# Optimization experiments

Measured on AMD Instinct MI355X. Metric: run time of the kernel, lower is better.

The kernel has to match this reference:

```python
import jax, jax.numpy as jnp
import numpy as np

B, D, L, H = 8192, 1024, 64, 256

def setup_inputs() -> dict:
    key = jax.random.key(0)
    k_x, k_w1, k_b1, k_w2, k_b2 = jax.random.split(key, 5)
    # Stacked per-label parameters (equivalent to L independent 2-layer MLPs)
    lim1 = 1.0 / np.sqrt(D)
    lim2 = 1.0 / np.sqrt(H)
    return {
        "x": jax.random.normal(k_x, (B, D), dtype=jnp.float32),
        "W1": jax.random.uniform(k_w1, (L, D, H), dtype=jnp.float32, minval=-lim1, maxval=lim1),
        "b1": jax.random.uniform(k_b1, (L, H), dtype=jnp.float32, minval=-lim1, maxval=lim1),
        "W2": jax.random.uniform(k_w2, (L, H), dtype=jnp.float32, minval=-lim2, maxval=lim2),
        "b2": jax.random.uniform(k_b2, (L,), dtype=jnp.float32, minval=-lim2, maxval=lim2),
    }

def reference(x, W1, b1, W2, b2):
    # h: [B, L, H] = relu(x @ W1_l + b1_l) for every label l, as one batched GEMM
    h = jax.nn.relu(jnp.einsum('bd,ldh->blh', x, W1) + b1[None, :, :])
    # out: [B, L] = h_l @ W2_l + b2_l  (second Linear has output dim 1, squeezed)
    out = jnp.einsum('blh,lh->bl', h, W2) + b2[None, :]
    return out
```

## Files before the change

kernel.cpp:

```cpp
#include <hip/hip_runtime.h>
#include <stdint.h>

#define B_SZ 8192
#define D_SZ 1024
#define L_SZ 64
#define H_SZ 256

#define BM 128
#define BN 256
#define BK 32
#define NTILE (D_SZ / BK)

typedef __attribute__((ext_vector_type(8))) __bf16 bf16x8;
typedef __attribute__((ext_vector_type(4))) float f32x4;

typedef __attribute__((address_space(1))) void as1_void;
typedef __attribute__((address_space(3))) void as3_void;

static __device__ __forceinline__ void gload_lds16(const void* g, void* l) {
    __builtin_amdgcn_global_load_lds((as1_void*)g, (as3_void*)l, 16, 0, 0);
}

static __device__ __forceinline__ unsigned short f2bf(float f) {
    uint32_t u = __builtin_bit_cast(uint32_t, f);
    u += 0x7fffu + ((u >> 16) & 1u);
    return (unsigned short)(u >> 16);
}

__global__ void cvt_x_kernel(const float* __restrict__ x, unsigned short* __restrict__ xb) {
    int i = blockIdx.x * blockDim.x + threadIdx.x;
    const float4 v = reinterpret_cast<const float4*>(x)[i];
    ushort4 o;
    o.x = f2bf(v.x); o.y = f2bf(v.y); o.z = f2bf(v.z); o.w = f2bf(v.w);
    reinterpret_cast<ushort4*>(xb)[i] = o;
}

__global__ void transpose_w1_kernel(const float* __restrict__ w1, unsigned short* __restrict__ w1t) {
    __shared__ float tile[64][65];
    int b = blockIdx.x;
    int l  = b >> 6;
    int dt = (b >> 2) & 15;
    int ht = b & 3;
    int tx = threadIdx.x & 63;
    int ty = threadIdx.x >> 6;
    const float* src = w1 + (size_t)l * (D_SZ * H_SZ);
    #pragma unroll
    for (int r = 0; r < 64; r += 4)
        tile[r + ty][tx] = src[(size_t)(dt * 64 + r + ty) * H_SZ + ht * 64 + tx];
    __syncthreads();
    unsigned short* dst = w1t + (size_t)l * (H_SZ * D_SZ);
    #pragma unroll
    for (int r = 0; r < 64; r += 4)
        dst[(size_t)(ht * 64 + r + ty) * D_SZ + dt * 64 + tx] = f2bf(tile[tx][r + ty]);
}


#define SBAR asm volatile("s_barrier" ::: "memory")
#define VMW(n) asm volatile("s_waitcnt vmcnt(" #n ")" ::: "memory")

#define STAGE(t, bi) do { \
    const size_t koff = (size_t)(t) * BK; \
    gload_lds16(aSrcG + koff,    (char*)&ldsA[bi][0] + tid * 16); \
    gload_lds16(bSrcG0 + koff,   (char*)&ldsB[bi][0] + tid * 16); \
    gload_lds16(bSrcG1 + koff,   (char*)&ldsB[bi][0] + 8192 + tid * 16); \
} while(0)

#define COMPUTE(bi) do { \
    bf16x8 af[4], bv[4]; \
    _Pragma("unroll") for (int m = 0; m < 4; ++m) { \
        const int row = wr * 64 + m * 16 + rl; \
        const int slot = gq ^ ((row >> 1) & 3); \
        af[m] = *reinterpret_cast<const bf16x8*>( \
            reinterpret_cast<const char*>(&ldsA[bi][0]) + row * 64 + slot * 16); \
    } \
    _Pragma("unroll") for (int n = 0; n < 4; ++n) { \
        const int row = wc * 64 + n * 16 + rl; \
        const int slot = gq ^ ((row >> 1) & 3); \
        bv[n] = *reinterpret_cast<const bf16x8*>( \
            reinterpret_cast<const char*>(&ldsB[bi][0]) + row * 64 + slot * 16); \
    } \
    __builtin_amdgcn_s_setprio(1); \
    _Pragma("unroll") for (int m = 0; m < 4; ++m) \
    _Pragma("unroll") for (int n = 0; n < 4; ++n) \
        acc[m][n] = __builtin_amdgcn_mfma_f32_16x16x32_bf16(af[m], bv[n], acc[m][n], 0, 0, 0); \
    __builtin_amdgcn_s_setprio(0); \
} while(0)

__global__ __launch_bounds__(512, 4) void ffn_gemm_kernel(
    const unsigned short* __restrict__ xb,
    const unsigned short* __restrict__ w1t,
    const float* __restrict__ b1,
    const float* __restrict__ w2,
    const float* __restrict__ b2,
    float* __restrict__ out)
{
    __shared__ unsigned short ldsA[3][BM * BK];
    __shared__ unsigned short ldsB[3][BN * BK];
    __shared__ float partLds[2][64][4];

    const int bid = blockIdx.x;
    const int wg  = ((bid & 7) << 9) + (bid >> 3);
    const int l   = wg >> 6;
    const int m0  = (wg & 63) * BM;

    const int tid  = threadIdx.x;
    const int wid  = tid >> 6;
    const int lane = tid & 63;
    const int wr   = wid >> 2;
    const int wc   = wid & 3;
    const int gq   = lane >> 4;
    const int rl   = lane & 15;

    const int arow = tid >> 2;
    const int aslt = tid & 3;
    const unsigned short* aSrcG =
        xb + (size_t)(m0 + arow) * D_SZ + (aslt ^ ((arow >> 1) & 3)) * 8;
    const int brow0 = tid >> 2;
    const unsigned short* bSrcG0 =
        w1t + ((size_t)l * H_SZ + brow0) * D_SZ + ((tid & 3) ^ ((brow0 >> 1) & 3)) * 8;
    const int q1 = 512 + tid;
    const int brow1 = q1 >> 2;
    const unsigned short* bSrcG1 =
        w1t + ((size_t)l * H_SZ + brow1) * D_SZ + ((q1 & 3) ^ ((brow1 >> 1) & 3)) * 8;

    f32x4 acc[4][4];
    #pragma unroll
    for (int m = 0; m < 4; ++m)
        #pragma unroll
        for (int n = 0; n < 4; ++n) {
            acc[m][n][0] = 0.f; acc[m][n][1] = 0.f;
            acc[m][n][2] = 0.f; acc[m][n][3] = 0.f;
        }

    STAGE(0, 0); STAGE(1, 1);
    VMW(3);
    SBAR;

    #pragma unroll 1
    for (int tt = 0; tt < 30; tt += 3) {
        STAGE(tt + 2, 2); VMW(6); SBAR; COMPUTE(0); SBAR;
        STAGE(tt + 3, 0); VMW(6); SBAR; COMPUTE(1); SBAR;
        STAGE(tt + 4, 1); VMW(6); SBAR; COMPUTE(2); SBAR;
    }
    VMW(3); SBAR; COMPUTE(0); SBAR;
    VMW(0); SBAR; COMPUTE(1);

    float b1v[4], w2v[4];
    #pragma unroll
    for (int n = 0; n < 4; ++n) {
        const int col = wc * 64 + n * 16 + rl;
        b1v[n] = b1[l * H_SZ + col];
        w2v[n] = w2[l * H_SZ + col];
    }
    const float b2v = b2[l];
    #pragma unroll
    for (int m = 0; m < 4; ++m) {
        #pragma unroll
        for (int r = 0; r < 4; ++r) {
            float p = 0.f;
            #pragma unroll
            for (int n = 0; n < 4; ++n) {
                float v = acc[m][n][r] + b1v[n];
                v = fmaxf(v, 0.f);
                p += v * w2v[n];
            }
            p += __shfl_xor(p, 1);
            p += __shfl_xor(p, 2);
            p += __shfl_xor(p, 4);
            p += __shfl_xor(p, 8);
            if (rl == 0)
                partLds[wr][m * 16 + gq * 4 + r][wc] = p;
        }
    }
    __syncthreads();
    if (tid < BM) {
        float s = b2v;
        #pragma unroll
        for (int w = 0; w < 4; ++w) s += partLds[tid >> 6][tid & 63][w];
        out[(size_t)(m0 + tid) * L_SZ + l] = s;
    }
}

extern "C" void kernel_launch(void* const* d_in, const int* in_sizes, int n_in,
                              void* d_out, int out_size, void* d_ws, size_t ws_size,
                              hipStream_t stream) {
    const float* x  = (const float*)d_in[0];
    const float* W1 = (const float*)d_in[1];
    const float* b1 = (const float*)d_in[2];
    const float* W2 = (const float*)d_in[3];
    const float* b2 = (const float*)d_in[4];
    float* out = (float*)d_out;

    unsigned short* xb  = (unsigned short*)d_ws;
    unsigned short* w1t = xb + (size_t)B_SZ * D_SZ;

    cvt_x_kernel<<<(B_SZ * D_SZ / 4) / 256, 256, 0, stream>>>(x, xb);
    transpose_w1_kernel<<<L_SZ * 16 * 4, 256, 0, stream>>>(W1, w1t);
    ffn_gemm_kernel<<<(B_SZ / BM) * L_SZ, 512, 0, stream>>>(xb, w1t, b1, W2, b2, out);
}
```

Before: 316.8 us.

## Double M tile to 256 and interleave LDS reads, staging and MFMA halves

```diff
diff --git a/kernel.cpp b/kernel.cpp
--- a/kernel.cpp
+++ b/kernel.cpp
@@ -6,10 +6,10 @@
 #define L_SZ 64
 #define H_SZ 256
 
-#define BM 128
+#define BM 256
 #define BN 256
 #define BK 32
-#define NTILE (D_SZ / BK)
+#define NT (D_SZ / BK)
 
 typedef __attribute__((ext_vector_type(8))) __bf16 bf16x8;
 typedef __attribute__((ext_vector_type(4))) float f32x4;
@@ -58,35 +58,43 @@
 #define SBAR asm volatile("s_barrier" ::: "memory")
 #define VMW(n) asm volatile("s_waitcnt vmcnt(" #n ")" ::: "memory")
 
-#define STAGE(t, bi) do { \
-    const size_t koff = (size_t)(t) * BK; \
-    gload_lds16(aSrcG + koff,    (char*)&ldsA[bi][0] + tid * 16); \
-    gload_lds16(bSrcG0 + koff,   (char*)&ldsB[bi][0] + tid * 16); \
-    gload_lds16(bSrcG1 + koff,   (char*)&ldsB[bi][0] + 8192 + tid * 16); \
-} while(0)
-
-#define COMPUTE(bi) do { \
-    bf16x8 af[4], bv[4]; \
+#define DS_A(cb, h) do { \
     _Pragma("unroll") for (int m = 0; m < 4; ++m) { \
-        const int row = wr * 64 + m * 16 + rl; \
-        const int slot = gq ^ ((row >> 1) & 3); \
+        const int row = wr * 128 + ((h) * 4 + m) * 16 + rl; \
+        const int slot = g ^ ((row >> 1) & 3); \
         af[m] = *reinterpret_cast<const bf16x8*>( \
-            reinterpret_cast<const char*>(&ldsA[bi][0]) + row * 64 + slot * 16); \
-    } \
+            reinterpret_cast<const char*>(&ldsA[cb][0]) + row * 64 + slot * 16); \
+    } } while(0)
+
+#define DS_B(cb) do { \
     _Pragma("unroll") for (int n = 0; n < 4; ++n) { \
         const int row = wc * 64 + n * 16 + rl; \
-        const int slot = gq ^ ((row >> 1) & 3); \
-        bv[n] = *reinterpret_cast<const bf16x8*>( \
-            reinterpret_cast<const char*>(&ldsB[bi][0]) + row * 64 + slot * 16); \
-    } \
+        const int slot = g ^ ((row >> 1) & 3); \
+        bfv[n] = *reinterpret_cast<const bf16x8*>( \
+            reinterpret_cast<const char*>(&ldsB[cb][0]) + row * 64 + slot * 16); \
+    } } while(0)
+
+#define MFMA_H(h) do { \
     __builtin_amdgcn_s_setprio(1); \
     _Pragma("unroll") for (int m = 0; m < 4; ++m) \
     _Pragma("unroll") for (int n = 0; n < 4; ++n) \
-        acc[m][n] = __builtin_amdgcn_mfma_f32_16x16x32_bf16(af[m], bv[n], acc[m][n], 0, 0, 0); \
-    __builtin_amdgcn_s_setprio(0); \
+        acc[(h) * 4 + m][n] = __builtin_amdgcn_mfma_f32_16x16x32_bf16( \
+            af[m], bfv[n], acc[(h) * 4 + m][n], 0, 0, 0); \
+    __builtin_amdgcn_s_setprio(0); } while(0)
+
+#define STAGE_A(t, sb) do { \
+    gload_lds16(aSrc[0] + (size_t)(t) * BK, (char*)&ldsA[sb][0] + tid * 16); \
+    gload_lds16(aSrc[1] + (size_t)(t) * BK, (char*)&ldsA[sb][0] + 8192 + tid * 16); } while(0)
+#define STAGE_B(t, sb) do { \
+    gload_lds16(bSrc[0] + (size_t)(t) * BK, (char*)&ldsB[sb][0] + tid * 16); \
+    gload_lds16(bSrc[1] + (size_t)(t) * BK, (char*)&ldsB[sb][0] + 8192 + tid * 16); } while(0)
+
+#define TILE(t, cb, sb) do { \
+    DS_A(cb, 0); DS_B(cb); STAGE_A((t) + 2, sb); SBAR; MFMA_H(0); SBAR; \
+    DS_A(cb, 1);           STAGE_B((t) + 2, sb); SBAR; MFMA_H(1); VMW(4); SBAR; \
 } while(0)
 
-__global__ __launch_bounds__(512, 4) void ffn_gemm_kernel(
+__global__ __launch_bounds__(512, 2) void ffn_gemm_kernel(
     const unsigned short* __restrict__ xb,
     const unsigned short* __restrict__ w1t,
     const float* __restrict__ b1,
@@ -96,87 +104,93 @@
 {
     __shared__ unsigned short ldsA[3][BM * BK];
     __shared__ unsigned short ldsB[3][BN * BK];
-    __shared__ float partLds[2][64][4];
+    __shared__ float partRed[256][4];
 
     const int bid = blockIdx.x;
-    const int wg  = ((bid & 7) << 9) + (bid >> 3);
-    const int l   = wg >> 6;
-    const int m0  = (wg & 63) * BM;
+    const int wg  = ((bid & 7) << 8) + (bid >> 3);
+    const int l   = wg >> 5;
+    const int m0  = (wg & 31) * BM;
 
     const int tid  = threadIdx.x;
     const int wid  = tid >> 6;
     const int lane = tid & 63;
     const int wr   = wid >> 2;
     const int wc   = wid & 3;
-    const int gq   = lane >> 4;
+    const int g    = lane >> 4;
     const int rl   = lane & 15;
 
-    const int arow = tid >> 2;
-    const int aslt = tid & 3;
-    const unsigned short* aSrcG =
-        xb + (size_t)(m0 + arow) * D_SZ + (aslt ^ ((arow >> 1) & 3)) * 8;
-    const int brow0 = tid >> 2;
-    const unsigned short* bSrcG0 =
-        w1t + ((size_t)l * H_SZ + brow0) * D_SZ + ((tid & 3) ^ ((brow0 >> 1) & 3)) * 8;
-    const int q1 = 512 + tid;
-    const int brow1 = q1 >> 2;
-    const unsigned short* bSrcG1 =
-        w1t + ((size_t)l * H_SZ + brow1) * D_SZ + ((q1 & 3) ^ ((brow1 >> 1) & 3)) * 8;
-
-    f32x4 acc[4][4];
-    #pragma unroll
-    for (int m = 0; m < 4; ++m)
+    const unsigned short* aSrc[2];
+    const unsigned short* bSrc[2];
+    #pragma unroll
+    for (int c2 = 0; c2 < 2; ++c2) {
+        const int q  = c2 * 512 + tid;
+        const int r  = q >> 2;
+        const int kg = (q & 3) ^ ((r >> 1) & 3);
+        aSrc[c2] = xb  + (size_t)(m0 + r) * D_SZ + kg * 8;
+        bSrc[c2] = w1t + ((size_t)l * H_SZ + r) * D_SZ + kg * 8;
+    }
+
+    float b1v[4], w2v[4];
+    #pragma unroll
+    for (int n = 0; n < 4; ++n) {
+        const int col = wc * 64 + n * 16 + rl;
+        b1v[n] = b1[l * H_SZ + col];
+        w2v[n] = w2[l * H_SZ + col];
+    }
+    const float b2v = b2[l];
+
+    f32x4 acc[8][4];
+    #pragma unroll
+    for (int m = 0; m < 8; ++m)
         #pragma unroll
         for (int n = 0; n < 4; ++n) {
             acc[m][n][0] = 0.f; acc[m][n][1] = 0.f;
             acc[m][n][2] = 0.f; acc[m][n][3] = 0.f;
         }
 
-    STAGE(0, 0); STAGE(1, 1);
-    VMW(3);
+    bf16x8 af[4], bfv[4];
+
+    STAGE_A(0, 0); STAGE_B(0, 0);
+    STAGE_A(1, 1); STAGE_B(1, 1);
+    VMW(4);
     SBAR;
 
     #pragma unroll 1
-    for (int tt = 0; tt < 30; tt += 3) {
-        STAGE(tt + 2, 2); VMW(6); SBAR; COMPUTE(0); SBAR;
-        STAGE(tt + 3, 0); VMW(6); SBAR; COMPUTE(1); SBAR;
-        STAGE(tt + 4, 1); VMW(6); SBAR; COMPUTE(2); SBAR;
-    }
-    VMW(3); SBAR; COMPUTE(0); SBAR;
-    VMW(0); SBAR; COMPUTE(1);
-
-    float b1v[4], w2v[4];
-    #pragma unroll
-    for (int n = 0; n < 4; ++n) {
-        const int col = wc * 64 + n * 16 + rl;
-        b1v[n] = b1[l * H_SZ + col];
-        w2v[n] = w2[l * H_SZ + col];
-    }
-    const float b2v = b2[l];
-    #pragma unroll
-    for (int m = 0; m < 4; ++m) {
+    for (int i = 0; i < 10; ++i) {
+        const int t = 3 * i;
+        TILE(t,     0, 2);
+        TILE(t + 1, 1, 0);
+        TILE(t + 2, 2, 1);
+    }
+    DS_A(0, 0); DS_B(0); SBAR; MFMA_H(0); SBAR;
+    DS_A(0, 1);          SBAR; MFMA_H(1); VMW(0); SBAR;
+    DS_A(1, 0); DS_B(1); SBAR; MFMA_H(0); SBAR;
+    DS_A(1, 1);          SBAR; MFMA_H(1);
+
+    #pragma unroll
+    for (int mf = 0; mf < 8; ++mf) {
         #pragma unroll
         for (int r = 0; r < 4; ++r) {
             float p = 0.f;
             #pragma unroll
-            for (int n = 0; n < 4; ++n) {
-                float v = acc[m][n][r] + b1v[n];
+            for (int nf = 0; nf < 4; ++nf) {
+                float v = acc[mf][nf][r] + b1v[nf];
                 v = fmaxf(v, 0.f);
-                p += v * w2v[n];
+                p += v * w2v[nf];
             }
             p += __shfl_xor(p, 1);
             p += __shfl_xor(p, 2);
             p += __shfl_xor(p, 4);
             p += __shfl_xor(p, 8);
             if (rl == 0)
-                partLds[wr][m * 16 + gq * 4 + r][wc] = p;
+                partRed[wr * 128 + mf * 16 + g * 4 + r][wc] = p;
         }
     }
     __syncthreads();
     if (tid < BM) {
         float s = b2v;
         #pragma unroll
-        for (int w = 0; w < 4; ++w) s += partLds[tid >> 6][tid & 63][w];
+        for (int w = 0; w < 4; ++w) s += partRed[tid][w];
         out[(size_t)(m0 + tid) * L_SZ + l] = s;
     }
 }
```

Result: slower. 339.8 us (+7.3%).
